# Performance work log

Measured on AMD Instinct MI355X. Metric: run time of the kernel, lower is better.

## Reference

```python
import jax, jax.numpy as jnp
import numpy as np

N_NODES = 50000
N_EDGES = 800000
D = 128          # node / edge / u feature dim
OUT = 128
N_GRAPHS = 64
IN1 = 4 * D      # 512
IN2 = D + OUT + D  # 384


def setup_inputs() -> dict:
    key = jax.random.key(0)
    ks = jax.random.split(key, 10)
    x = jax.random.normal(ks[0], (N_NODES, D), dtype=jnp.float32)
    edge_index = jax.random.randint(ks[1], (2, N_EDGES), 0, N_NODES, dtype=jnp.int64)
    edge_attr = jax.random.normal(ks[2], (N_EDGES, D), dtype=jnp.float32)
    u = jax.random.normal(ks[3], (N_GRAPHS, D), dtype=jnp.float32)
    batch = jnp.sort(jax.random.randint(ks[4], (N_NODES,), 0, N_GRAPHS, dtype=jnp.int64))
    # MLP params (Linear: y = x @ W.T + b), kaiming-ish scale
    W1 = jax.random.normal(ks[5], (OUT, IN1), dtype=jnp.float32) / np.sqrt(IN1)
    b1 = jnp.zeros((OUT,), dtype=jnp.float32)
    W2 = jax.random.normal(ks[6], (OUT, IN2), dtype=jnp.float32) / np.sqrt(IN2)
    b2 = jnp.zeros((OUT,), dtype=jnp.float32)
    return {"x": x, "edge_index": edge_index, "edge_attr": edge_attr,
            "u": u, "batch": batch, "W1": W1, "b1": b1, "W2": W2, "b2": b2}


def reference(x, edge_index, edge_attr, u, batch, W1, b1, W2, b2):
    src, dst = edge_index[0], edge_index[1]
    source_features = x[src]                  # [E, D]
    dest_features = x[dst]                    # [E, D]
    u_edge = u[batch[dst]]                    # [E, D]
    edge_input = jnp.concatenate([dest_features, source_features, edge_attr, u_edge], axis=1)  # [E, IN1]
    edge_messages = jax.nn.relu(edge_input @ W1.T + b1)  # [E, OUT]
    aggregated = jax.ops.segment_sum(edge_messages, dst, num_segments=x.shape[0])  # [N, OUT]
    u_expanded = u[batch]                     # [N, D]
    node_input = jnp.concatenate([x, aggregated, u_expanded], axis=1)  # [N, IN2]
    return jax.nn.relu(node_input @ W2.T + b2)  # [N, OUT]
```

## Files before the change

### kernel.cpp

```cpp
#include <hip/hip_runtime.h>
#include <stdint.h>

#define NNODES 50000
#define NEDGES 800000
#define DIM 128
#define IN1 512
#define IN2 384
#define NSB 196

typedef __attribute__((ext_vector_type(8))) short bf16x8;
typedef __attribute__((ext_vector_type(8))) unsigned short u16x8;
typedef __attribute__((ext_vector_type(4))) float f32x4;
typedef __attribute__((ext_vector_type(4))) uint32_t u32x4;
typedef __attribute__((ext_vector_type(2))) uint32_t u32x2;

__device__ __forceinline__ unsigned short f2bf(float f) {
  union { float f; uint32_t u; } v; v.f = f;
  return (unsigned short)((v.u + 0x7FFFu + ((v.u >> 16) & 1u)) >> 16);
}
__device__ __forceinline__ float bf2f(unsigned short u) {
  union { uint32_t u; float f; } v; v.u = ((uint32_t)u) << 16;
  return v.f;
}
__device__ __forceinline__ uint32_t cvtpk(float lo, float hi) {
  uint32_t r;
  asm volatile("v_cvt_pk_bf16_f32 %0, %1, %2" : "=v"(r) : "v"(lo), "v"(hi));
  return r;
}

__device__ __forceinline__ void cvt8(const float* __restrict__ p, unsigned short* dst, int sidx) {
  float4 f0 = *(const float4*)(p);
  float4 f1 = *(const float4*)(p + 4);
  u16x8 o;
  o[0] = f2bf(f0.x); o[1] = f2bf(f0.y); o[2] = f2bf(f0.z); o[3] = f2bf(f0.w);
  o[4] = f2bf(f1.x); o[5] = f2bf(f1.y); o[6] = f2bf(f1.z); o[7] = f2bf(f1.w);
  *(u16x8*)(dst + sidx) = o;
}

__device__ __forceinline__ void mfma128(const unsigned short* As, const unsigned short* Bs,
                                        f32x4 acc[4][4], int wm, int wn, int l) {
#pragma unroll
  for (int kk = 0; kk < 4; ++kk) {
    bf16x8 a[4], b[4];
#pragma unroll
    for (int mi = 0; mi < 4; ++mi) {
      int row = wm * 64 + mi * 16 + (l & 15);
      int idx = (row * 128 + kk * 32 + (l >> 4) * 8) ^ ((row & 7) << 3);
      a[mi] = *(const bf16x8*)(As + idx);
    }
#pragma unroll
    for (int ni = 0; ni < 4; ++ni) {
      int nrow = wn * 64 + ni * 16 + (l & 15);
      int idx = (nrow * 128 + kk * 32 + (l >> 4) * 8) ^ ((nrow & 7) << 3);
      b[ni] = *(const bf16x8*)(Bs + idx);
    }
#pragma unroll
    for (int mi = 0; mi < 4; ++mi)
#pragma unroll
      for (int ni = 0; ni < 4; ++ni)
        acc[mi][ni] = __builtin_amdgcn_mfma_f32_16x16x32_bf16(a[mi], b[ni], acc[mi][ni], 0, 0, 0);
  }
}

__global__ void zero_kernel(float4* __restrict__ a, int n4, int* __restrict__ c, int nc) {
  int i = blockIdx.x * 256 + threadIdx.x;
  int stride = gridDim.x * 256;
  for (int k = i; k < n4; k += stride) a[k] = float4{0.f, 0.f, 0.f, 0.f};
  for (int k = i; k < nc; k += stride) c[k] = 0;
}

__global__ void wconv_p0_kernel(const float* __restrict__ W1, const float* __restrict__ W2,
                                const float* __restrict__ u, const float* __restrict__ b1,
                                const float* __restrict__ b2,
                                unsigned short* __restrict__ Wt,
                                float* __restrict__ Ud, float* __restrict__ Uc) {
  int b = blockIdx.x;
  if (b < 320) {
    int t = b * 256 + threadIdx.x;
    int tile = t >> 14, rem = t & 16383, n = rem >> 7, k = rem & 127;
    float v = (tile < 3) ? W1[(size_t)n * IN1 + tile * 128 + k]
                         : W2[(size_t)n * IN2 + (tile - 3) * 128 + k];
    int lin = ((n * 128 + (k & ~7)) ^ ((n & 7) << 3)) | (k & 7);
    Wt[tile * 16384 + lin] = f2bf(v);
  } else {
    int g = (b - 320) * 2 + (threadIdx.x >> 7);
    int c = threadIdx.x & 127;
    const float* ur = u + (size_t)g * DIM;
    const float* w1 = W1 + (size_t)c * IN1 + 384;
    const float* w2 = W2 + (size_t)c * IN2 + 256;
    float s1 = b1[c], s2 = b2[c];
    for (int k = 0; k < DIM; ++k) { float uv = ur[k]; s1 += uv * w1[k]; s2 += uv * w2[k]; }
    Ud[g * DIM + c] = s1;
    Uc[g * DIM + c] = s2;
  }
}

__global__ __launch_bounds__(256, 2) void p1_kernel(
    const float* __restrict__ x, const int* __restrict__ batch,
    const unsigned short* __restrict__ Wt,
    const float* __restrict__ Ud, const float* __restrict__ Uc,
    unsigned short* __restrict__ Xad, unsigned short* __restrict__ Xb,
    unsigned short* __restrict__ Yx) {
  __shared__ __align__(16) unsigned short As[128 * 128];
  __shared__ __align__(16) unsigned short Bs[128 * 128];
  const int t = threadIdx.x, l = t & 63, w = t >> 6, wm = w >> 1, wn = w & 1;
  const int n0 = blockIdx.x * 128;
#pragma unroll
  for (int i = 0; i < 16; ++i) {
    int idx = i * 256 + t;
    int row = idx >> 5;
    int c = (idx & 31) * 4;
    int n = n0 + row; if (n >= NNODES) n = NNODES - 1;
    float4 f = *(const float4*)(x + (size_t)n * DIM + c);
    u32x2 g = {cvtpk(f.x, f.y), cvtpk(f.z, f.w)};
    *(u32x2*)(As + (row * 128 + (c ^ ((row & 7) << 3)))) = g;
  }
#pragma unroll
  for (int p = 0; p < 3; ++p) {
    __syncthreads();
    {
      const u16x8* wsrc = (const u16x8*)(Wt + (size_t)((p == 2) ? 3 : p) * 16384);
      u16x8* bdst = (u16x8*)Bs;
#pragma unroll
      for (int i = 0; i < 8; ++i) bdst[t + i * 256] = wsrc[t + i * 256];
    }
    __syncthreads();
    f32x4 acc[4][4] = {};
    mfma128(As, Bs, acc, wm, wn, l);
#pragma unroll
    for (int mi = 0; mi < 4; ++mi)
#pragma unroll
      for (int rr = 0; rr < 4; ++rr) {
        int m = wm * 64 + mi * 16 + (l >> 4) * 4 + rr;
        int n = n0 + m;
        if (n < NNODES) {
          int g = batch[n];
#pragma unroll
          for (int ni = 0; ni < 4; ++ni) {
            int col = wn * 64 + ni * 16 + (l & 15);
            float v = acc[mi][ni][rr];
            if (p == 0)      Xad[(size_t)n * DIM + col] = f2bf(v + Ud[g * DIM + col]);
            else if (p == 1) Xb [(size_t)n * DIM + col] = f2bf(v);
            else             Yx [(size_t)n * DIM + col] = f2bf(v + Uc[g * DIM + col]);
          }
        }
      }
  }
}

__global__ void hist_kernel(const int* __restrict__ dstI, int* __restrict__ count) {
  int e = blockIdx.x * 256 + threadIdx.x;
  if (e < NEDGES) atomicAdd(&count[dstI[e]], 1);
}

__global__ void scan1_kernel(const int* __restrict__ count, int* __restrict__ bsum) {
  __shared__ int ws[4];
  int i = blockIdx.x * 256 + threadIdx.x;
  int v = (i < NNODES) ? count[i] : 0;
  int l = threadIdx.x & 63;
#pragma unroll
  for (int off = 32; off > 0; off >>= 1) v += __shfl_down(v, off);
  if (l == 0) ws[threadIdx.x >> 6] = v;
  __syncthreads();
  if (threadIdx.x == 0) bsum[blockIdx.x] = ws[0] + ws[1] + ws[2] + ws[3];
}

__global__ void scan2_kernel(const int* __restrict__ bsum, int* __restrict__ bpre) {
  __shared__ int s[256];
  int i = threadIdx.x;
  int v = (i < NSB) ? bsum[i] : 0;
  s[i] = v; __syncthreads();
  for (int off = 1; off < 256; off <<= 1) {
    int u = (i >= off) ? s[i - off] : 0;
    __syncthreads();
    s[i] += u;
    __syncthreads();
  }
  if (i < NSB) bpre[i] = s[i] - v;
}

__global__ void scan3_kernel(const int* __restrict__ count, const int* __restrict__ bpre,
                             int* __restrict__ rowptr) {
  __shared__ int s[256];
  int b = blockIdx.x, i = threadIdx.x, g = b * 256 + i;
  int v = (g < NNODES) ? count[g] : 0;
  s[i] = v; __syncthreads();
  for (int off = 1; off < 256; off <<= 1) {
    int u = (i >= off) ? s[i - off] : 0;
    __syncthreads();
    s[i] += u;
    __syncthreads();
  }
  if (g < NNODES) rowptr[g] = bpre[b] + s[i] - v;
}

__global__ void scatter_kernel(const int* __restrict__ srcI, const int* __restrict__ dstI,
                               int* __restrict__ rowptr, uint64_t* __restrict__ esd) {
  int e = blockIdx.x * 256 + threadIdx.x;
  if (e < NEDGES) {
    int d = dstI[e], s = srcI[e];
    int pos = atomicAdd(&rowptr[d], 1);
    esd[pos] = ((uint64_t)(uint32_t)e << 32) | ((uint32_t)s << 16) | (uint32_t)d;
  }
}

__global__ __launch_bounds__(512, 6) void edge2_kernel(
    const float* __restrict__ ea, const uint64_t* __restrict__ esd,
    const unsigned short* __restrict__ W1cs,
    const unsigned short* __restrict__ Xad, const unsigned short* __restrict__ Xb,
    float* __restrict__ agg) {
  __shared__ __align__(16) unsigned short smem[24576];
  __shared__ int dlds[64];
  __shared__ int segs[66];
  __shared__ int nsegS;
  unsigned short* As  = smem;
  unsigned short* Bs  = smem + 8192;
  unsigned short* Xbs = smem;
  float* Ms = (float*)(smem + 8192);

  const int t = threadIdx.x, l = t & 63, w = t >> 6;
  const int wm = w >> 2, wn = w & 3;
  int bid = blockIdx.x;
  const int nwg = NEDGES / 64, q = nwg >> 3, r8 = nwg & 7;
  int xcd = bid & 7, off = bid >> 3;
  int wg = (xcd < r8) ? xcd * (q + 1) + off : r8 * (q + 1) + (xcd - r8) * q + off;
  const int p0 = wg * 64;
  const int r = t >> 3, o = t & 7;
  const int swz = (r & 7) << 3;

  {
    const u16x8* wsrc = (const u16x8*)W1cs;
    u16x8* bdst = (u16x8*)Bs;
#pragma unroll
    for (int i = 0; i < 4; ++i) bdst[t + i * 512] = wsrc[t + i * 512];
  }
  uint64_t v = esd[p0 + r];
  if (o == 0) dlds[r] = (int)(v & 0xFFFF);
  {
    int e = (int)(v >> 32);
    const float* rowp = ea + (size_t)e * DIM + o * 4;
    float4 f0 = *(const float4*)(rowp);
    float4 f1 = *(const float4*)(rowp + 32);
    float4 f2 = *(const float4*)(rowp + 64);
    float4 f3 = *(const float4*)(rowp + 96);
    u32x2 g0 = {cvtpk(f0.x, f0.y), cvtpk(f0.z, f0.w)};
    u32x2 g1 = {cvtpk(f1.x, f1.y), cvtpk(f1.z, f1.w)};
    u32x2 g2 = {cvtpk(f2.x, f2.y), cvtpk(f2.z, f2.w)};
    u32x2 g3 = {cvtpk(f3.x, f3.y), cvtpk(f3.z, f3.w)};
    *(u32x2*)(As + (r * 128 + ((o * 4      ) ^ swz))) = g0;
    *(u32x2*)(As + (r * 128 + ((o * 4 +  32) ^ swz))) = g1;
    *(u32x2*)(As + (r * 128 + ((o * 4 +  64) ^ swz))) = g2;
    *(u32x2*)(As + (r * 128 + ((o * 4 +  96) ^ swz))) = g3;
  }
  u16x8 x0, x1;
  {
    int s = (int)((v >> 16) & 0xFFFF);
    const u16x8* xr = (const u16x8*)(Xb + (size_t)s * DIM);
    x0 = xr[o];
    x1 = xr[o + 8];
  }
  __syncthreads();

  if (w == 0) {
    int d = dlds[l];
    int dp = __shfl_up(d, 1);
    bool st = (l == 0) || (d != dp);
    uint64_t m = __ballot(st);
    int rank = (l == 0) ? 0 : __popcll(m & ((1ull << l) - 1ull));
    if (st) segs[rank] = l;
    if (l == 0) { int ns = __popcll(m); nsegS = ns; segs[ns] = 64; }
  }

  f32x4 acc[2][2] = {};
#pragma unroll
  for (int kk = 0; kk < 4; ++kk) {
    bf16x8 a[2], b[2];
#pragma unroll
    for (int mi = 0; mi < 2; ++mi) {
      int row = wm * 32 + mi * 16 + (l & 15);
      int idx = (row * 128 + kk * 32 + (l >> 4) * 8) ^ ((row & 7) << 3);
      a[mi] = *(const bf16x8*)(As + idx);
    }
#pragma unroll
    for (int ni = 0; ni < 2; ++ni) {
      int n = wn * 32 + ni * 16 + (l & 15);
      int idx = (n * 128 + kk * 32 + (l >> 4) * 8) ^ ((n & 7) << 3);
      b[ni] = *(const bf16x8*)(Bs + idx);
    }
#pragma unroll
    for (int mi = 0; mi < 2; ++mi)
#pragma unroll
      for (int ni = 0; ni < 2; ++ni)
        acc[mi][ni] = __builtin_amdgcn_mfma_f32_16x16x32_bf16(a[mi], b[ni], acc[mi][ni], 0, 0, 0);
  }
  __syncthreads();

  {
    int cx = ((r >> 2) & 3) << 4;
    *(u16x8*)(Xbs + (r * 128 + ((o * 8     ) ^ cx))) = x0;
    *(u16x8*)(Xbs + (r * 128 + ((o * 8 + 64) ^ cx))) = x1;
  }
  __syncthreads();

#pragma unroll
  for (int mi = 0; mi < 2; ++mi)
#pragma unroll
    for (int rr = 0; rr < 4; ++rr) {
      int m = wm * 32 + mi * 16 + (l >> 4) * 4 + rr;
      int d = dlds[m];
      const unsigned short* xa = Xad + (size_t)d * DIM;
      int cs = ((m >> 2) & 3) << 3;
      int cx = ((m >> 2) & 3) << 4;
#pragma unroll
      for (int ni = 0; ni < 2; ++ni) {
        int col = wn * 32 + ni * 16 + (l & 15);
        float vv = acc[mi][ni][rr] + bf2f(xa[col]) + bf2f(Xbs[m * 128 + (col ^ cx)]);
        Ms[m * 128 + (col ^ cs)] = fmaxf(vv, 0.0f);
      }
    }
  __syncthreads();

  {
    int nseg = nsegS;
    for (int sc = w; sc < nseg; sc += 8) {
      int beg = segs[sc], end = segs[sc + 1];
      int d = dlds[beg];
      float* arow = agg + (size_t)d * DIM;
      bool interior = (sc > 0) && (sc < nseg - 1);
#pragma unroll
      for (int cc = 0; cc < 2; ++cc) {
        int col = l + cc * 64;
        float s = 0.0f;
        for (int r2 = beg; r2 < end; ++r2)
          s += Ms[r2 * 128 + (col ^ (((r2 >> 2) & 3) << 3))];
        if (interior) arow[col] = s;
        else unsafeAtomicAdd(arow + col, s);
      }
    }
  }
}

__global__ __launch_bounds__(256, 2) void edge_kernel(
    const float* __restrict__ ea, const int* __restrict__ srcI, const int* __restrict__ dstI,
    const unsigned short* __restrict__ W1cs,
    const unsigned short* __restrict__ Xad, const unsigned short* __restrict__ Xb,
    float* __restrict__ agg) {
  __shared__ __align__(16) unsigned short As[128 * 128];
  __shared__ __align__(16) unsigned short Bs[128 * 128];
  const int t = threadIdx.x, l = t & 63, w = t >> 6, wm = w >> 1, wn = w & 1;
  const int e0 = blockIdx.x * 128, r = t >> 1, h = t & 1;
  const int swz = (r & 7) << 3;
  {
    const float* rowp = ea + (size_t)(e0 + r) * DIM + h * 64;
#pragma unroll
    for (int i = 0; i < 8; ++i) cvt8(rowp + i * 8, As, (r * 128 + h * 64 + i * 8) ^ swz);
  }
  {
    const u16x8* wsrc = (const u16x8*)W1cs;
    u16x8* bdst = (u16x8*)Bs;
#pragma unroll
    for (int i = 0; i < 8; ++i) bdst[t + i * 256] = wsrc[t + i * 256];
  }
  __syncthreads();
  f32x4 acc[4][4] = {};
  mfma128(As, Bs, acc, wm, wn, l);
#pragma unroll
  for (int mi = 0; mi < 4; ++mi)
#pragma unroll
    for (int rr = 0; rr < 4; ++rr) {
      int m = wm * 64 + mi * 16 + (l >> 4) * 4 + rr;
      int e = e0 + m;
      int d = dstI[e], s = srcI[e];
      const unsigned short* xa = Xad + (size_t)d * DIM;
      const unsigned short* xb = Xb + (size_t)s * DIM;
      float* ag = agg + (size_t)d * DIM;
#pragma unroll
      for (int ni = 0; ni < 4; ++ni) {
        int col = wn * 64 + ni * 16 + (l & 15);
        float v = acc[mi][ni][rr] + bf2f(xa[col]) + bf2f(xb[col]);
        unsafeAtomicAdd(ag + col, fmaxf(v, 0.0f));
      }
    }
}

__global__ __launch_bounds__(256, 2) void node_kernel(
    const float* __restrict__ agg, const unsigned short* __restrict__ Wt,
    const unsigned short* __restrict__ Yx, float* __restrict__ out) {
  __shared__ __align__(16) unsigned short As[128 * 128];
  __shared__ __align__(16) unsigned short Bs[128 * 128];
  const int t = threadIdx.x, l = t & 63, w = t >> 6, wm = w >> 1, wn = w & 1;
  const int n0 = blockIdx.x * 128;
#pragma unroll
  for (int i = 0; i < 16; ++i) {
    int idx = i * 256 + t;
    int row = idx >> 5;
    int c = (idx & 31) * 4;
    int n = n0 + row; if (n >= NNODES) n = NNODES - 1;
    float4 f = *(const float4*)(agg + (size_t)n * DIM + c);
    u32x2 g = {cvtpk(f.x, f.y), cvtpk(f.z, f.w)};
    *(u32x2*)(As + (row * 128 + (c ^ ((row & 7) << 3)))) = g;
  }
  {
    const u16x8* wsrc = (const u16x8*)(Wt + (size_t)4 * 16384);
    u16x8* bdst = (u16x8*)Bs;
#pragma unroll
    for (int i = 0; i < 8; ++i) bdst[t + i * 256] = wsrc[t + i * 256];
  }
  __syncthreads();
  f32x4 acc[4][4] = {};
  mfma128(As, Bs, acc, wm, wn, l);
#pragma unroll
  for (int mi = 0; mi < 4; ++mi)
#pragma unroll
    for (int rr = 0; rr < 4; ++rr) {
      int m = wm * 64 + mi * 16 + (l >> 4) * 4 + rr;
      int n = n0 + m;
      if (n < NNODES) {
        float* orow = out + (size_t)n * DIM;
#pragma unroll
        for (int ni = 0; ni < 4; ++ni) {
          int col = wn * 64 + ni * 16 + (l & 15);
          float v = acc[mi][ni][rr] + bf2f(Yx[(size_t)n * DIM + col]);
          orow[col] = fmaxf(v, 0.0f);
        }
      }
    }
}

extern "C" void kernel_launch(void* const* d_in, const int* in_sizes, int n_in,
                              void* d_out, int out_size, void* d_ws, size_t ws_size,
                              hipStream_t stream) {
  const float* x   = (const float*)d_in[0];
  const int* ei    = (const int*)d_in[1];
  const float* ea  = (const float*)d_in[2];
  const float* u   = (const float*)d_in[3];
  const int* batch = (const int*)d_in[4];
  const float* W1  = (const float*)d_in[5];
  const float* b1  = (const float*)d_in[6];
  const float* W2  = (const float*)d_in[7];
  const float* b2  = (const float*)d_in[8];
  float* out = (float*)d_out;
  const int* srcI = ei;
  const int* dstI = ei + NEDGES;

  const size_t XAD_B = (size_t)NNODES * DIM * 2;
  const size_t U_B   = (size_t)64 * DIM * 4;
  const size_t WT_B  = (size_t)5 * 16384 * 2;
  const size_t ESD_B = (size_t)NEDGES * 8;
  const size_t CNT_B = (size_t)(NNODES + 64) * 4;
  const size_t BS_B  = 4096;
  const size_t need_base = 3 * XAD_B + 2 * U_B + WT_B;
  const size_t need_sort = need_base + ESD_B + 2 * CNT_B + 2 * BS_B;

  char* p = (char*)d_ws;
  unsigned short* Xad = (unsigned short*)p; p += XAD_B;
  unsigned short* Xb  = (unsigned short*)p; p += XAD_B;
  unsigned short* Yx  = (unsigned short*)p; p += XAD_B;
  float* Ud = (float*)p; p += U_B;
  float* Uc = (float*)p; p += U_B;
  unsigned short* Wt = (unsigned short*)p; p += WT_B;
  uint64_t* esd = (uint64_t*)p; p += ESD_B;
  int* count  = (int*)p; p += CNT_B;
  int* rowptr = (int*)p; p += CNT_B;
  int* bsum = (int*)p; p += BS_B;
  int* bpre = (int*)p;

  float* agg = out;
  const int nAgg4 = NNODES * DIM / 4;

  if (ws_size >= need_sort) {
    zero_kernel<<<2048, 256, 0, stream>>>((float4*)agg, nAgg4, count, NNODES + 64);
    hist_kernel<<<(NEDGES + 255) / 256, 256, 0, stream>>>(dstI, count);
    scan1_kernel<<<NSB, 256, 0, stream>>>(count, bsum);
    scan2_kernel<<<1, 256, 0, stream>>>(bsum, bpre);
    scan3_kernel<<<NSB, 256, 0, stream>>>(count, bpre, rowptr);
    scatter_kernel<<<(NEDGES + 255) / 256, 256, 0, stream>>>(srcI, dstI, rowptr, esd);
    wconv_p0_kernel<<<352, 256, 0, stream>>>(W1, W2, u, b1, b2, Wt, Ud, Uc);
    p1_kernel<<<(NNODES + 127) / 128, 256, 0, stream>>>(x, batch, Wt, Ud, Uc, Xad, Xb, Yx);
    edge2_kernel<<<NEDGES / 64, 512, 0, stream>>>(ea, esd, Wt + 2 * 16384, Xad, Xb, agg);
    node_kernel<<<(NNODES + 127) / 128, 256, 0, stream>>>(agg, Wt, Yx, out);
  } else if (ws_size >= need_base) {
    zero_kernel<<<2048, 256, 0, stream>>>((float4*)agg, nAgg4, (int*)Ud, 0);
    wconv_p0_kernel<<<352, 256, 0, stream>>>(W1, W2, u, b1, b2, Wt, Ud, Uc);
    p1_kernel<<<(NNODES + 127) / 128, 256, 0, stream>>>(x, batch, Wt, Ud, Uc, Xad, Xb, Yx);
    edge_kernel<<<NEDGES / 128, 256, 0, stream>>>(ea, srcI, dstI, Wt + 2 * 16384, Xad, Xb, agg);
    node_kernel<<<(NNODES + 127) / 128, 256, 0, stream>>>(agg, Wt, Yx, out);
  }
}
```

Baseline: 311.2 us.

## Restructure edge kernel into per-wave streaming over 64 edges with running segment sums

Replaces the 64-edge, 512-thread edge kernel with a 256-thread kernel in which each wave handles 64 sorted edges in four 16-edge steps. Edge-attribute fragments are loaded straight into MFMA A registers, and each wave computes the full 128 output columns. Each wave uses its own LDS tile, so block barriers inside the loop are gone. Aggregation keeps running per-destination sums across steps, so only a segment touching the chunk boundary needs an atomic. The W1 tile load is now shared by 256 edges instead of 64; in exchange, occupancy is lower and intermediate messages are rounded to bf16 in LDS.

```diff
diff --git a/kernel.cpp b/kernel.cpp
--- a/kernel.cpp
+++ b/kernel.cpp
@@ -204,139 +204,118 @@
   }
 }
 
-__global__ __launch_bounds__(512, 6) void edge2_kernel(
+__global__ __launch_bounds__(256, 3) void edge3_kernel(
     const float* __restrict__ ea, const uint64_t* __restrict__ esd,
     const unsigned short* __restrict__ W1cs,
     const unsigned short* __restrict__ Xad, const unsigned short* __restrict__ Xb,
     float* __restrict__ agg) {
-  __shared__ __align__(16) unsigned short smem[24576];
-  __shared__ int dlds[64];
-  __shared__ int segs[66];
-  __shared__ int nsegS;
-  unsigned short* As  = smem;
-  unsigned short* Bs  = smem + 8192;
-  unsigned short* Xbs = smem;
-  float* Ms = (float*)(smem + 8192);
+  __shared__ __align__(16) unsigned short Bs[16384];
+  __shared__ __align__(16) unsigned short Ms[4][2048];
+  __shared__ int dlds[4][16];
 
   const int t = threadIdx.x, l = t & 63, w = t >> 6;
-  const int wm = w >> 2, wn = w & 3;
   int bid = blockIdx.x;
-  const int nwg = NEDGES / 64, q = nwg >> 3, r8 = nwg & 7;
+  const int nwg = NEDGES / 256, q = nwg >> 3, r8 = nwg & 7;
   int xcd = bid & 7, off = bid >> 3;
   int wg = (xcd < r8) ? xcd * (q + 1) + off : r8 * (q + 1) + (xcd - r8) * q + off;
-  const int p0 = wg * 64;
-  const int r = t >> 3, o = t & 7;
-  const int swz = (r & 7) << 3;
+  const int ebase = wg * 256 + w * 64;
 
   {
     const u16x8* wsrc = (const u16x8*)W1cs;
     u16x8* bdst = (u16x8*)Bs;
 #pragma unroll
-    for (int i = 0; i < 4; ++i) bdst[t + i * 512] = wsrc[t + i * 512];
-  }
-  uint64_t v = esd[p0 + r];
-  if (o == 0) dlds[r] = (int)(v & 0xFFFF);
-  {
-    int e = (int)(v >> 32);
-    const float* rowp = ea + (size_t)e * DIM + o * 4;
-    float4 f0 = *(const float4*)(rowp);
-    float4 f1 = *(const float4*)(rowp + 32);
-    float4 f2 = *(const float4*)(rowp + 64);
-    float4 f3 = *(const float4*)(rowp + 96);
-    u32x2 g0 = {cvtpk(f0.x, f0.y), cvtpk(f0.z, f0.w)};
-    u32x2 g1 = {cvtpk(f1.x, f1.y), cvtpk(f1.z, f1.w)};
-    u32x2 g2 = {cvtpk(f2.x, f2.y), cvtpk(f2.z, f2.w)};
-    u32x2 g3 = {cvtpk(f3.x, f3.y), cvtpk(f3.z, f3.w)};
-    *(u32x2*)(As + (r * 128 + ((o * 4      ) ^ swz))) = g0;
-    *(u32x2*)(As + (r * 128 + ((o * 4 +  32) ^ swz))) = g1;
-    *(u32x2*)(As + (r * 128 + ((o * 4 +  64) ^ swz))) = g2;
-    *(u32x2*)(As + (r * 128 + ((o * 4 +  96) ^ swz))) = g3;
-  }
-  u16x8 x0, x1;
-  {
-    int s = (int)((v >> 16) & 0xFFFF);
-    const u16x8* xr = (const u16x8*)(Xb + (size_t)s * DIM);
-    x0 = xr[o];
-    x1 = xr[o + 8];
+    for (int i = 0; i < 8; ++i) bdst[t + i * 256] = wsrc[t + i * 256];
   }
   __syncthreads();
 
-  if (w == 0) {
-    int d = dlds[l];
-    int dp = __shfl_up(d, 1);
-    bool st = (l == 0) || (d != dp);
-    uint64_t m = __ballot(st);
-    int rank = (l == 0) ? 0 : __popcll(m & ((1ull << l) - 1ull));
-    if (st) segs[rank] = l;
-    if (l == 0) { int ns = __popcll(m); nsegS = ns; segs[ns] = 64; }
-  }
-
-  f32x4 acc[2][2] = {};
-#pragma unroll
-  for (int kk = 0; kk < 4; ++kk) {
-    bf16x8 a[2], b[2];
-#pragma unroll
-    for (int mi = 0; mi < 2; ++mi) {
-      int row = wm * 32 + mi * 16 + (l & 15);
-      int idx = (row * 128 + kk * 32 + (l >> 4) * 8) ^ ((row & 7) << 3);
-      a[mi] = *(const bf16x8*)(As + idx);
-    }
-#pragma unroll
-    for (int ni = 0; ni < 2; ++ni) {
-      int n = wn * 32 + ni * 16 + (l & 15);
-      int idx = (n * 128 + kk * 32 + (l >> 4) * 8) ^ ((n & 7) << 3);
-      b[ni] = *(const bf16x8*)(Bs + idx);
-    }
-#pragma unroll
-    for (int mi = 0; mi < 2; ++mi)
-#pragma unroll
-      for (int ni = 0; ni < 2; ++ni)
-        acc[mi][ni] = __builtin_amdgcn_mfma_f32_16x16x32_bf16(a[mi], b[ni], acc[mi][ni], 0, 0, 0);
-  }
-  __syncthreads();
-
-  {
-    int cx = ((r >> 2) & 3) << 4;
-    *(u16x8*)(Xbs + (r * 128 + ((o * 8     ) ^ cx))) = x0;
-    *(u16x8*)(Xbs + (r * 128 + ((o * 8 + 64) ^ cx))) = x1;
-  }
-  __syncthreads();
-
-#pragma unroll
-  for (int mi = 0; mi < 2; ++mi)
+  unsigned short* ms = Ms[w];
+  int* dl = dlds[w];
+  const int row = l & 15, g = l >> 4;
+  const int c0 = l, c1 = l + 64;
+
+  int curd = -1, curbeg = 0;
+  float sum0 = 0.f, sum1 = 0.f;
+
+  for (int it = 0; it < 4; ++it) {
+    const int p0 = ebase + it * 16;
+    uint64_t ev = 0;
+    if (l < 16) ev = esd[p0 + l];
+    int e_l = (int)(ev >> 32);
+    int s_l = (int)((ev >> 16) & 0xFFFF);
+    if (l < 16) dl[l] = (int)(ev & 0xFFFF);
+    int e = __shfl(e_l, row);
+    int s = __shfl(s_l, row);
+
+    const float* ap = ea + (size_t)e * DIM + g * 8;
+    bf16x8 afr[4];
+#pragma unroll
+    for (int kk = 0; kk < 4; ++kk) {
+      float4 f0 = *(const float4*)(ap + kk * 32);
+      float4 f1 = *(const float4*)(ap + kk * 32 + 4);
+      union { u32x4 u; bf16x8 b; } cv;
+      cv.u = (u32x4){cvtpk(f0.x, f0.y), cvtpk(f0.z, f0.w), cvtpk(f1.x, f1.y), cvtpk(f1.z, f1.w)};
+      afr[kk] = cv.b;
+    }
+
+    {
+      const unsigned short* xr = Xb + (size_t)s * DIM + g * 32;
+      int sw = (row & 7) << 3;
+#pragma unroll
+      for (int i = 0; i < 4; ++i) {
+        u16x8 xv = *(const u16x8*)(xr + i * 8);
+        *(u16x8*)(ms + row * 128 + ((g * 32 + i * 8) ^ sw)) = xv;
+      }
+    }
+
+    f32x4 acc[8] = {};
+#pragma unroll
+    for (int kk = 0; kk < 4; ++kk) {
+#pragma unroll
+      for (int ni = 0; ni < 8; ++ni) {
+        int n = row + ni * 16;
+        int idx = (n * 128 + kk * 32 + g * 8) ^ ((n & 7) << 3);
+        bf16x8 b = *(const bf16x8*)(Bs + idx);
+        acc[ni] = __builtin_amdgcn_mfma_f32_16x16x32_bf16(afr[kk], b, acc[ni], 0, 0, 0);
+      }
+    }
+
 #pragma unroll
     for (int rr = 0; rr < 4; ++rr) {
-      int m = wm * 32 + mi * 16 + (l >> 4) * 4 + rr;
-      int d = dlds[m];
+      int m = g * 4 + rr;
+      int d = dl[m];
       const unsigned short* xa = Xad + (size_t)d * DIM;
-      int cs = ((m >> 2) & 3) << 3;
-      int cx = ((m >> 2) & 3) << 4;
-#pragma unroll
-      for (int ni = 0; ni < 2; ++ni) {
-        int col = wn * 32 + ni * 16 + (l & 15);
-        float vv = acc[mi][ni][rr] + bf2f(xa[col]) + bf2f(Xbs[m * 128 + (col ^ cx)]);
-        Ms[m * 128 + (col ^ cs)] = fmaxf(vv, 0.0f);
-      }
-    }
-  __syncthreads();
-
-  {
-    int nseg = nsegS;
-    for (int sc = w; sc < nseg; sc += 8) {
-      int beg = segs[sc], end = segs[sc + 1];
-      int d = dlds[beg];
-      float* arow = agg + (size_t)d * DIM;
-      bool interior = (sc > 0) && (sc < nseg - 1);
-#pragma unroll
-      for (int cc = 0; cc < 2; ++cc) {
-        int col = l + cc * 64;
-        float s = 0.0f;
-        for (int r2 = beg; r2 < end; ++r2)
-          s += Ms[r2 * 128 + (col ^ (((r2 >> 2) & 3) << 3))];
-        if (interior) arow[col] = s;
-        else unsafeAtomicAdd(arow + col, s);
-      }
-    }
+      int sw = (m & 7) << 3;
+#pragma unroll
+      for (int ni = 0; ni < 8; ++ni) {
+        int n = row + ni * 16;
+        int idx = m * 128 + (n ^ sw);
+        float vv = acc[ni][rr] + bf2f(xa[n]) + bf2f(ms[idx]);
+        ms[idx] = f2bf(fmaxf(vv, 0.f));
+      }
+    }
+
+    for (int i = 0; i < 16; ++i) {
+      int d = dl[i];
+      int sw = (i & 7) << 3;
+      float v0 = bf2f(ms[i * 128 + (c0 ^ sw)]);
+      float v1 = bf2f(ms[i * 128 + (c1 ^ sw)]);
+      int gi = it * 16 + i;
+      if (d != curd) {
+        if (curd >= 0) {
+          float* arow = agg + (size_t)curd * DIM;
+          if (curbeg > 0) { arow[c0] = sum0; arow[c1] = sum1; }
+          else { unsafeAtomicAdd(arow + c0, sum0); unsafeAtomicAdd(arow + c1, sum1); }
+        }
+        curd = d; curbeg = gi; sum0 = v0; sum1 = v1;
+      } else {
+        sum0 += v0; sum1 += v1;
+      }
+    }
+  }
+  if (curd >= 0) {
+    float* arow = agg + (size_t)curd * DIM;
+    unsafeAtomicAdd(arow + c0, sum0);
+    unsafeAtomicAdd(arow + c1, sum1);
   }
 }
 
@@ -477,7 +456,7 @@
     scatter_kernel<<<(NEDGES + 255) / 256, 256, 0, stream>>>(srcI, dstI, rowptr, esd);
     wconv_p0_kernel<<<352, 256, 0, stream>>>(W1, W2, u, b1, b2, Wt, Ud, Uc);
     p1_kernel<<<(NNODES + 127) / 128, 256, 0, stream>>>(x, batch, Wt, Ud, Uc, Xad, Xb, Yx);
-    edge2_kernel<<<NEDGES / 64, 512, 0, stream>>>(ea, esd, Wt + 2 * 16384, Xad, Xb, agg);
+    edge3_kernel<<<NEDGES / 256, 256, 0, stream>>>(ea, esd, Wt + 2 * 16384, Xad, Xb, agg);
     node_kernel<<<(NNODES + 127) / 128, 256, 0, stream>>>(agg, Wt, Yx, out);
   } else if (ws_size >= need_base) {
     zero_kernel<<<2048, 256, 0, stream>>>((float4*)agg, nAgg4, (int*)Ud, 0);
```

Measured after the change: 424.5 us. +36.4%, slower.

## Make edge kernel persistent over ten tiles with prefetched gathers

Applied to the files above, without the earlier changes.

The edge kernel now processes ten 64-edge tiles per workgroup in a loop. It loads the W1 slice into shared memory once per workgroup instead of once per tile, and prefetches the next tile's edge_attr rows, source features and sort indices while the current tile is in MFMA and reduce. Barriers wait only on LDS counters so in-flight global loads are not drained. The message tile is also stored as bf16 instead of fp32 to save LDS, which adds rounding error to the segment sums. The launch grid shrinks tenfold and the occupancy hint drops from 6 to 4, which risks fewer waves to hide latency.

```diff
diff --git a/kernel.cpp b/kernel.cpp
--- a/kernel.cpp
+++ b/kernel.cpp
@@ -7,12 +7,20 @@
 #define IN1 512
 #define IN2 384
 #define NSB 196
+#define PT 10
 
 typedef __attribute__((ext_vector_type(8))) short bf16x8;
 typedef __attribute__((ext_vector_type(8))) unsigned short u16x8;
 typedef __attribute__((ext_vector_type(4))) float f32x4;
 typedef __attribute__((ext_vector_type(4))) uint32_t u32x4;
 typedef __attribute__((ext_vector_type(2))) uint32_t u32x2;
+
+#define BARRIER_NODRAIN() do {                       \
+    __builtin_amdgcn_sched_barrier(0);               \
+    asm volatile("s_waitcnt lgkmcnt(0)");            \
+    __builtin_amdgcn_s_barrier();                    \
+    __builtin_amdgcn_sched_barrier(0);               \
+  } while (0)
 
 __device__ __forceinline__ unsigned short f2bf(float f) {
   union { float f; uint32_t u; } v; v.f = f;
@@ -204,29 +212,29 @@
   }
 }
 
-__global__ __launch_bounds__(512, 6) void edge2_kernel(
+__global__ __launch_bounds__(512, 4) void edge4_kernel(
     const float* __restrict__ ea, const uint64_t* __restrict__ esd,
     const unsigned short* __restrict__ W1cs,
     const unsigned short* __restrict__ Xad, const unsigned short* __restrict__ Xb,
     float* __restrict__ agg) {
-  __shared__ __align__(16) unsigned short smem[24576];
-  __shared__ int dlds[64];
-  __shared__ int segs[66];
-  __shared__ int nsegS;
-  unsigned short* As  = smem;
-  unsigned short* Bs  = smem + 8192;
-  unsigned short* Xbs = smem;
-  float* Ms = (float*)(smem + 8192);
+  __shared__ __align__(16) unsigned short Bs[16384];
+  __shared__ __align__(16) unsigned short As[8192];
+  __shared__ __align__(16) unsigned short Xbs[8192];
+  __shared__ int dlds[2][64];
+  __shared__ int segs[2][66];
+  __shared__ int nsegS[2];
+  unsigned short* Ms = As;
 
   const int t = threadIdx.x, l = t & 63, w = t >> 6;
   const int wm = w >> 2, wn = w & 3;
   int bid = blockIdx.x;
-  const int nwg = NEDGES / 64, q = nwg >> 3, r8 = nwg & 7;
+  const int nwg = NEDGES / (64 * PT), q = nwg >> 3, r8_ = nwg & 7;
   int xcd = bid & 7, off = bid >> 3;
-  int wg = (xcd < r8) ? xcd * (q + 1) + off : r8 * (q + 1) + (xcd - r8) * q + off;
-  const int p0 = wg * 64;
+  int wg = (xcd < r8_) ? xcd * (q + 1) + off : r8_ * (q + 1) + (xcd - r8_) * q + off;
+  const int base = wg * (64 * PT);
   const int r = t >> 3, o = t & 7;
   const int swz = (r & 7) << 3;
+  const int cxr = ((r >> 2) & 3) << 4;
 
   {
     const u16x8* wsrc = (const u16x8*)W1cs;
@@ -234,109 +242,127 @@
 #pragma unroll
     for (int i = 0; i < 4; ++i) bdst[t + i * 512] = wsrc[t + i * 512];
   }
-  uint64_t v = esd[p0 + r];
-  if (o == 0) dlds[r] = (int)(v & 0xFFFF);
-  {
-    int e = (int)(v >> 32);
-    const float* rowp = ea + (size_t)e * DIM + o * 4;
-    float4 f0 = *(const float4*)(rowp);
-    float4 f1 = *(const float4*)(rowp + 32);
-    float4 f2 = *(const float4*)(rowp + 64);
-    float4 f3 = *(const float4*)(rowp + 96);
-    u32x2 g0 = {cvtpk(f0.x, f0.y), cvtpk(f0.z, f0.w)};
-    u32x2 g1 = {cvtpk(f1.x, f1.y), cvtpk(f1.z, f1.w)};
-    u32x2 g2 = {cvtpk(f2.x, f2.y), cvtpk(f2.z, f2.w)};
-    u32x2 g3 = {cvtpk(f3.x, f3.y), cvtpk(f3.z, f3.w)};
-    *(u32x2*)(As + (r * 128 + ((o * 4      ) ^ swz))) = g0;
-    *(u32x2*)(As + (r * 128 + ((o * 4 +  32) ^ swz))) = g1;
-    *(u32x2*)(As + (r * 128 + ((o * 4 +  64) ^ swz))) = g2;
-    *(u32x2*)(As + (r * 128 + ((o * 4 +  96) ^ swz))) = g3;
-  }
+
+  uint64_t v0 = esd[base + r];
+  uint64_t vn = esd[base + 64 + r];
+  uint64_t vn2 = esd[base + 128 + r];
+  float4 a0, a1, a2, a3;
   u16x8 x0, x1;
   {
-    int s = (int)((v >> 16) & 0xFFFF);
+    int e = (int)(v0 >> 32);
+    const float* rowp = ea + (size_t)e * DIM + o * 4;
+    a0 = *(const float4*)(rowp);
+    a1 = *(const float4*)(rowp + 32);
+    a2 = *(const float4*)(rowp + 64);
+    a3 = *(const float4*)(rowp + 96);
+    int s = (int)((v0 >> 16) & 0xFFFF);
     const u16x8* xr = (const u16x8*)(Xb + (size_t)s * DIM);
-    x0 = xr[o];
-    x1 = xr[o + 8];
-  }
-  __syncthreads();
-
-  if (w == 0) {
-    int d = dlds[l];
-    int dp = __shfl_up(d, 1);
-    bool st = (l == 0) || (d != dp);
-    uint64_t m = __ballot(st);
-    int rank = (l == 0) ? 0 : __popcll(m & ((1ull << l) - 1ull));
-    if (st) segs[rank] = l;
-    if (l == 0) { int ns = __popcll(m); nsegS = ns; segs[ns] = 64; }
-  }
-
-  f32x4 acc[2][2] = {};
-#pragma unroll
-  for (int kk = 0; kk < 4; ++kk) {
-    bf16x8 a[2], b[2];
-#pragma unroll
-    for (int mi = 0; mi < 2; ++mi) {
-      int row = wm * 32 + mi * 16 + (l & 15);
-      int idx = (row * 128 + kk * 32 + (l >> 4) * 8) ^ ((row & 7) << 3);
-      a[mi] = *(const bf16x8*)(As + idx);
-    }
-#pragma unroll
-    for (int ni = 0; ni < 2; ++ni) {
-      int n = wn * 32 + ni * 16 + (l & 15);
-      int idx = (n * 128 + kk * 32 + (l >> 4) * 8) ^ ((n & 7) << 3);
-      b[ni] = *(const bf16x8*)(Bs + idx);
-    }
+    x0 = xr[o]; x1 = xr[o + 8];
+  }
+
+  for (int tt = 0; tt < PT; ++tt) {
+    const int cur = tt & 1;
+    if (o == 0) dlds[cur][r] = (int)(v0 & 0xFFFF);
+    {
+      u32x2 g0 = {cvtpk(a0.x, a0.y), cvtpk(a0.z, a0.w)};
+      u32x2 g1 = {cvtpk(a1.x, a1.y), cvtpk(a1.z, a1.w)};
+      u32x2 g2 = {cvtpk(a2.x, a2.y), cvtpk(a2.z, a2.w)};
+      u32x2 g3 = {cvtpk(a3.x, a3.y), cvtpk(a3.z, a3.w)};
+      *(u32x2*)(As + (r * 128 + ((o * 4     ) ^ swz))) = g0;
+      *(u32x2*)(As + (r * 128 + ((o * 4 + 32) ^ swz))) = g1;
+      *(u32x2*)(As + (r * 128 + ((o * 4 + 64) ^ swz))) = g2;
+      *(u32x2*)(As + (r * 128 + ((o * 4 + 96) ^ swz))) = g3;
+      *(u16x8*)(Xbs + (r * 128 + ((o * 8     ) ^ cxr))) = x0;
+      *(u16x8*)(Xbs + (r * 128 + ((o * 8 + 64) ^ cxr))) = x1;
+    }
+    if (tt < PT - 1) {
+      int e = (int)(vn >> 32);
+      const float* rowp = ea + (size_t)e * DIM + o * 4;
+      a0 = *(const float4*)(rowp);
+      a1 = *(const float4*)(rowp + 32);
+      a2 = *(const float4*)(rowp + 64);
+      a3 = *(const float4*)(rowp + 96);
+      int s = (int)((vn >> 16) & 0xFFFF);
+      const u16x8* xr = (const u16x8*)(Xb + (size_t)s * DIM);
+      x0 = xr[o]; x1 = xr[o + 8];
+    }
+    v0 = vn; vn = vn2;
+    {
+      int nidx = (tt + 3 < PT) ? (base + (tt + 3) * 64 + r) : (base + r);
+      vn2 = esd[nidx];
+    }
+    BARRIER_NODRAIN();
+
+    if (w == 0) {
+      int d = dlds[cur][l];
+      int dp = __shfl_up(d, 1);
+      bool st = (l == 0) || (d != dp);
+      uint64_t m = __ballot(st);
+      int rank = (l == 0) ? 0 : __popcll(m & ((1ull << l) - 1ull));
+      if (st) segs[cur][rank] = l;
+      if (l == 0) { int ns = __popcll(m); nsegS[cur] = ns; segs[cur][ns] = 64; }
+    }
+
+    f32x4 acc[2][2] = {};
+#pragma unroll
+    for (int kk = 0; kk < 4; ++kk) {
+      bf16x8 a[2], b[2];
+#pragma unroll
+      for (int mi = 0; mi < 2; ++mi) {
+        int row = wm * 32 + mi * 16 + (l & 15);
+        int idx = (row * 128 + kk * 32 + (l >> 4) * 8) ^ ((row & 7) << 3);
+        a[mi] = *(const bf16x8*)(As + idx);
+      }
+#pragma unroll
+      for (int ni = 0; ni < 2; ++ni) {
+        int n = wn * 32 + ni * 16 + (l & 15);
+        int idx = (n * 128 + kk * 32 + (l >> 4) * 8) ^ ((n & 7) << 3);
+        b[ni] = *(const bf16x8*)(Bs + idx);
+      }
+#pragma unroll
+      for (int mi = 0; mi < 2; ++mi)
+#pragma unroll
+        for (int ni = 0; ni < 2; ++ni)
+          acc[mi][ni] = __builtin_amdgcn_mfma_f32_16x16x32_bf16(a[mi], b[ni], acc[mi][ni], 0, 0, 0);
+    }
+    BARRIER_NODRAIN();
+
 #pragma unroll
     for (int mi = 0; mi < 2; ++mi)
 #pragma unroll
-      for (int ni = 0; ni < 2; ++ni)
-        acc[mi][ni] = __builtin_amdgcn_mfma_f32_16x16x32_bf16(a[mi], b[ni], acc[mi][ni], 0, 0, 0);
-  }
-  __syncthreads();
-
-  {
-    int cx = ((r >> 2) & 3) << 4;
-    *(u16x8*)(Xbs + (r * 128 + ((o * 8     ) ^ cx))) = x0;
-    *(u16x8*)(Xbs + (r * 128 + ((o * 8 + 64) ^ cx))) = x1;
-  }
-  __syncthreads();
-
-#pragma unroll
-  for (int mi = 0; mi < 2; ++mi)
-#pragma unroll
-    for (int rr = 0; rr < 4; ++rr) {
-      int m = wm * 32 + mi * 16 + (l >> 4) * 4 + rr;
-      int d = dlds[m];
-      const unsigned short* xa = Xad + (size_t)d * DIM;
-      int cs = ((m >> 2) & 3) << 3;
-      int cx = ((m >> 2) & 3) << 4;
-#pragma unroll
-      for (int ni = 0; ni < 2; ++ni) {
-        int col = wn * 32 + ni * 16 + (l & 15);
-        float vv = acc[mi][ni][rr] + bf2f(xa[col]) + bf2f(Xbs[m * 128 + (col ^ cx)]);
-        Ms[m * 128 + (col ^ cs)] = fmaxf(vv, 0.0f);
-      }
-    }
-  __syncthreads();
-
-  {
-    int nseg = nsegS;
-    for (int sc = w; sc < nseg; sc += 8) {
-      int beg = segs[sc], end = segs[sc + 1];
-      int d = dlds[beg];
-      float* arow = agg + (size_t)d * DIM;
-      bool interior = (sc > 0) && (sc < nseg - 1);
-#pragma unroll
-      for (int cc = 0; cc < 2; ++cc) {
-        int col = l + cc * 64;
-        float s = 0.0f;
-        for (int r2 = beg; r2 < end; ++r2)
-          s += Ms[r2 * 128 + (col ^ (((r2 >> 2) & 3) << 3))];
-        if (interior) arow[col] = s;
-        else unsafeAtomicAdd(arow + col, s);
-      }
-    }
+      for (int rr = 0; rr < 4; ++rr) {
+        int m = wm * 32 + mi * 16 + (l >> 4) * 4 + rr;
+        int d = dlds[cur][m];
+        const unsigned short* xa = Xad + (size_t)d * DIM;
+        int cx = ((m >> 2) & 3) << 4;
+#pragma unroll
+        for (int ni = 0; ni < 2; ++ni) {
+          int col = wn * 32 + ni * 16 + (l & 15);
+          float vv = acc[mi][ni][rr] + bf2f(xa[col]) + bf2f(Xbs[m * 128 + (col ^ cx)]);
+          Ms[m * 128 + (col ^ cx)] = f2bf(fmaxf(vv, 0.f));
+        }
+      }
+    BARRIER_NODRAIN();
+
+    {
+      int nseg = nsegS[cur];
+      for (int sc = w; sc < nseg; sc += 8) {
+        int beg = segs[cur][sc], end = segs[cur][sc + 1];
+        int d = dlds[cur][beg];
+        float* arow = agg + (size_t)d * DIM;
+        bool interior = (sc > 0) && (sc < nseg - 1);
+#pragma unroll
+        for (int cc = 0; cc < 2; ++cc) {
+          int col = l + cc * 64;
+          float s = 0.0f;
+          for (int r2 = beg; r2 < end; ++r2)
+            s += bf2f(Ms[r2 * 128 + (col ^ (((r2 >> 2) & 3) << 4))]);
+          if (interior) arow[col] = s;
+          else unsafeAtomicAdd(arow + col, s);
+        }
+      }
+    }
+    BARRIER_NODRAIN();
   }
 }
 
@@ -477,7 +503,7 @@
     scatter_kernel<<<(NEDGES + 255) / 256, 256, 0, stream>>>(srcI, dstI, rowptr, esd);
     wconv_p0_kernel<<<352, 256, 0, stream>>>(W1, W2, u, b1, b2, Wt, Ud, Uc);
     p1_kernel<<<(NNODES + 127) / 128, 256, 0, stream>>>(x, batch, Wt, Ud, Uc, Xad, Xb, Yx);
-    edge2_kernel<<<NEDGES / 64, 512, 0, stream>>>(ea, esd, Wt + 2 * 16384, Xad, Xb, agg);
+    edge4_kernel<<<NEDGES / (64 * PT), 512, 0, stream>>>(ea, esd, Wt + 2 * 16384, Xad, Xb, agg);
     node_kernel<<<(NNODES + 127) / 128, 256, 0, stream>>>(agg, Wt, Yx, out);
   } else if (ws_size >= need_base) {
     zero_kernel<<<2048, 256, 0, stream>>>((float4*)agg, nAgg4, (int*)Ud, 0);
```

Measured after the change: 403.5 us. +29.7%, slower.
